# Optimization experiments

Measured on AMD Instinct MI355X. Metric: run time of the kernel, lower is better.

Reference implementation:

```python
import jax, jax.numpy as jnp
import numpy as np

NUM_EMBEDDINGS = 1024
EMBEDDING_DIM = 256
COMMITMENT_COST = 1.0


def setup_inputs() -> dict:
    key = jax.random.key(0)
    k_in, k_emb = jax.random.split(key)
    inputs = jax.random.normal(k_in, (64, 32, 32, EMBEDDING_DIM), dtype=jnp.float32)
    embeddings = jax.random.normal(k_emb, (NUM_EMBEDDINGS, EMBEDDING_DIM), dtype=jnp.float32)
    return {"inputs": inputs, "embeddings": embeddings}


def reference(inputs, embeddings):
    # Eval-mode forward of VectorQuantizerEMA (EMA buffer update is a no-grad
    # stateful side effect, skipped here; see notes).
    input_shape = inputs.shape
    flat = inputs.reshape(-1, EMBEDDING_DIM)                       # [N, D]
    distances = (
        jnp.sum(flat ** 2, axis=1, keepdims=True)
        + jnp.sum(embeddings ** 2, axis=1)
        - 2.0 * flat @ embeddings.T
    )
    encoding_indices = jnp.argmin(distances, axis=1)               # [N]
    # one-hot @ embeddings == gather (avoid materializing [N, K] one-hot)
    quantized = embeddings[encoding_indices].reshape(input_shape)
    e_latent_loss = jnp.mean((jax.lax.stop_gradient(quantized) - inputs) ** 2)
    loss = COMMITMENT_COST * e_latent_loss
    # straight-through estimator
    quantized_st = inputs + jax.lax.stop_gradient(quantized - inputs)
    return quantized_st, loss, encoding_indices[:, None]
```

## Files before the change

### kernel.cpp

```cpp
#include <hip/hip_runtime.h>
#include <float.h>

#define NROWS 65536
#define DK 256
#define NCODES 1024
#define FLAG_CAP 8192
#define MARGIN1 0.15f
#define D_BIAS 384.0f

#define LOSS_OFF 16777216
#define IDX_OFF  16777217

#define CHUNK_STRIDE 1040

#define WS_FLAG1   0
#define WS_LOSSP   8
#define WS_ENORMD  520
#define WS_ENORMF  8720
#define WS_FROWS   12816
#define WS_IDX     45584
#define WS_EHI     307728
#define WS_ET      307728

typedef _Float16 f16x8 __attribute__((ext_vector_type(8)));
typedef float f32x4 __attribute__((ext_vector_type(4)));
typedef unsigned int uint32;

__device__ __forceinline__ uint32 packh2(float a, float b) {
  return (uint32)__builtin_bit_cast(unsigned short, (_Float16)a) |
         ((uint32)__builtin_bit_cast(unsigned short, (_Float16)b) << 16);
}

__global__ __launch_bounds__(256) void init_kernel(
    const float* __restrict__ E, double* __restrict__ enorm_d,
    float* __restrict__ enorm_f, uint4* __restrict__ Ehi,
    int* __restrict__ flag1, double* __restrict__ loss_part) {
  const int t = threadIdx.x;
  const int c = blockIdx.x * 8 + (t >> 5);
  const int g = t & 31;
  if (blockIdx.x == 0) {
    if (t == 0) *flag1 = 0;
    if (t < 64) loss_part[t] = 0.0;
  }
  const float4* er4 = (const float4*)(E + (size_t)c * DK);
  const float4 va = er4[g * 2];
  const float4 vb = er4[g * 2 + 1];
  double s = (double)va.x * va.x + (double)va.y * va.y + (double)va.z * va.z + (double)va.w * va.w
           + (double)vb.x * vb.x + (double)vb.y * vb.y + (double)vb.z * vb.z + (double)vb.w * vb.w;
  uint4 h;
  h.x = packh2(va.x, va.y);
  h.y = packh2(va.z, va.w);
  h.z = packh2(vb.x, vb.y);
  h.w = packh2(vb.z, vb.w);
  const int ctg = c >> 8, cga = (c >> 4) & 15, col = c & 15;
  const int kc = g >> 2, quad = g & 3;
  Ehi[((size_t)((ctg * 8 + kc) * 16 + cga)) * 64 + (size_t)(quad * 16 + col)] = h;
  #pragma unroll
  for (int m = 1; m < 32; m <<= 1) s += __shfl_xor(s, m, 64);
  if (g == 0) {
    enorm_d[c] = s;
    enorm_f[c] = (float)s;
  }
}

__global__ __launch_bounds__(256, 3) void dist_core(
    const float* __restrict__ X, const uint4* __restrict__ Ehi,
    const float* __restrict__ enorm_f, int* __restrict__ idx_ws,
    int* __restrict__ flag1, int* __restrict__ flag_rows,
    float* __restrict__ out) {
  __shared__ __attribute__((aligned(16))) char lds[33280];
  const int tid = threadIdx.x;
  const int lane = tid & 63;
  const int wid = tid >> 6;
  const int col = lane & 15;
  const int rowBase = blockIdx.x * 64;

  {
    const float4* X4 = (const float4*)X + (size_t)rowBase * 64;
    #pragma unroll
    for (int i = 0; i < 16; ++i) {
      const int f4 = i * 256 + tid;
      const int row = f4 >> 6;
      const int k0 = (f4 & 63) << 2;
      const float4 v = X4[f4];
      uint2 p;
      p.x = packh2(v.x, v.y);
      p.y = packh2(v.z, v.w);
      const int chunk = (row >> 4) * 8 + (k0 >> 5);
      const int off = chunk * CHUNK_STRIDE
                      + (((k0 >> 3) & 3) * 16 + (row & 15)) * 16
                      + ((k0 >> 2) & 1) * 8;
      *(uint2*)(lds + off) = p;
    }
  }
  __syncthreads();

  float rv1[16], rv2[16];
  #pragma unroll
  for (int i = 0; i < 16; ++i) { rv1[i] = FLT_MAX; rv2[i] = FLT_MAX; }

  f32x4 acc[4][4];
  #pragma unroll
  for (int rg = 0; rg < 4; ++rg)
    #pragma unroll
    for (int cg = 0; cg < 4; ++cg) acc[rg][cg] = (f32x4){0.f, 0.f, 0.f, 0.f};

  f16x8 bhA[4], bhB[4];
  auto loadB_ = [&](int t, f16x8* bh) {
    const size_t ub = ((size_t)(t * 16 + wid * 4)) * 64 + (size_t)lane;
    #pragma unroll
    for (int cg = 0; cg < 4; ++cg) bh[cg] = *(const f16x8*)&Ehi[ub + (size_t)cg * 64];
  };
  auto loadA_ = [&](int t, f16x8* av) {
    const int ks = t & 7;
    #pragma unroll
    for (int rg = 0; rg < 4; ++rg)
      av[rg] = *(const f16x8*)(lds + (rg * 8 + ks) * CHUNK_STRIDE + lane * 16);
  };
  auto domfma = [&](f16x8* av, f16x8* bh) {
    #pragma unroll
    for (int rg = 0; rg < 4; ++rg)
      #pragma unroll
      for (int cg = 0; cg < 4; ++cg)
        acc[rg][cg] = __builtin_amdgcn_mfma_f32_16x16x32_f16(av[rg], bh[cg], acc[rg][cg], 0, 0, 0);
  };
  auto epilogue = [&](int ctg) {
    #pragma unroll
    for (int cg = 0; cg < 4; ++cg) {
      const int code = ctg * 256 + wid * 64 + cg * 16 + col;
      const float en = enorm_f[code] + D_BIAS;
      const uint32 li = (uint32)((ctg << 6) | (cg << 4) | col);
      #pragma unroll
      for (int rg = 0; rg < 4; ++rg)
        #pragma unroll
        for (int reg = 0; reg < 4; ++reg) {
          const int i = rg * 4 + reg;
          const float dd = fmaf(-2.0f, acc[rg][cg][reg], en);
          const float p = __builtin_bit_cast(float,
              (__builtin_bit_cast(uint32, dd) & 0xFFFFFF00u) | li);
          rv2[i] = __builtin_amdgcn_fmed3f(p, rv1[i], rv2[i]);
          rv1[i] = fminf(rv1[i], p);
        }
    }
    #pragma unroll
    for (int rg = 0; rg < 4; ++rg)
      #pragma unroll
      for (int cg = 0; cg < 4; ++cg) acc[rg][cg] = (f32x4){0.f, 0.f, 0.f, 0.f};
  };

  loadB_(0, bhA);
  f16x8 av[4];
  for (int tt = 0; tt < 32; tt += 2) {
    loadB_(tt + 1, bhB);
    loadA_(tt, av);
    domfma(av, bhA);
    if (tt + 2 < 32) loadB_(tt + 2, bhA);
    loadA_(tt + 1, av);
    domfma(av, bhB);
    if (((tt + 1) & 7) == 7) epilogue(tt >> 3);
  }

  #pragma unroll
  for (int i = 0; i < 16; ++i) {
    #pragma unroll
    for (int m = 1; m < 16; m <<= 1) {
      const float o1 = __shfl_xor(rv1[i], m, 64);
      const float o2 = __shfl_xor(rv2[i], m, 64);
      rv2[i] = fminf(fminf(rv2[i], o2), fmaxf(rv1[i], o1));
      rv1[i] = fminf(rv1[i], o1);
    }
  }

  __syncthreads();
  float* M = (float*)lds;
  if (col == 0) {
    const int quad = lane >> 4;
    #pragma unroll
    for (int i = 0; i < 16; ++i) {
      const int row = (i >> 2) * 16 + quad * 4 + (i & 3);
      M[(row * 4 + wid) * 2 + 0] = rv1[i];
      M[(row * 4 + wid) * 2 + 1] = rv2[i];
    }
  }
  __syncthreads();
  if (tid < 64) {
    const float a1 = M[(tid * 4 + 0) * 2], a2 = M[(tid * 4 + 0) * 2 + 1];
    const float b1 = M[(tid * 4 + 1) * 2], b2 = M[(tid * 4 + 1) * 2 + 1];
    const float c1 = M[(tid * 4 + 2) * 2], c2 = M[(tid * 4 + 2) * 2 + 1];
    const float d1 = M[(tid * 4 + 3) * 2], d2 = M[(tid * 4 + 3) * 2 + 1];
    const float lo1 = fminf(a1, b1), hi1 = fmaxf(a1, b1);
    const float lo2 = fminf(c1, d1), hi2 = fmaxf(c1, d1);
    const float r1 = fminf(lo1, lo2);
    const float s1 = fminf(fmaxf(lo1, lo2), fminf(hi1, hi2));
    const float r2 = fminf(fminf(fminf(a2, b2), fminf(c2, d2)), s1);
    const int w1 = (r1 == a1) ? 0 : (r1 == b1) ? 1 : (r1 == c1) ? 2 : 3;
    const uint32 u1 = __builtin_bit_cast(uint32, r1);
    const int li = (int)(u1 & 255u);
    const int code = ((li >> 6) & 3) * 256 + w1 * 64 + ((li >> 4) & 3) * 16 + (li & 15);
    const int row = rowBase + tid;
    idx_ws[row] = code;
    out[IDX_OFF + row] = (float)code;
    const float q1 = __builtin_bit_cast(float, u1 & 0xFFFFFF00u);
    const float q2 = __builtin_bit_cast(float, __builtin_bit_cast(uint32, r2) & 0xFFFFFF00u);
    if (q2 - q1 < MARGIN1) {
      const int p = atomicAdd(flag1, 1);
      if (p < FLAG_CAP) flag_rows[p] = row;
    }
  }
}

__global__ __launch_bounds__(256) void gather_out(
    const float* __restrict__ X, const float* __restrict__ E,
    const int* __restrict__ idx_ws, float* __restrict__ out,
    double* __restrict__ loss_part) {
  const int lane = threadIdx.x & 63;
  const int wid = threadIdx.x >> 6;
  const int gw = blockIdx.x * 4 + wid;
  const int nw = gridDim.x * 4;
  double ls = 0.0;
  #pragma unroll 2
  for (int row = gw; row < NROWS; row += nw) {
    const int idx = idx_ws[row];
    const float4 q = ((const float4*)E)[(size_t)idx * 64 + lane];
    const float4 x = ((const float4*)X)[(size_t)row * 64 + lane];
    ((float4*)out)[(size_t)row * 64 + lane] = q;
    const double d0 = (double)q.x - (double)x.x;
    const double d1 = (double)q.y - (double)x.y;
    const double d2 = (double)q.z - (double)x.z;
    const double d3 = (double)q.w - (double)x.w;
    ls += d0 * d0 + d1 * d1 + d2 * d2 + d3 * d3;
  }
  #pragma unroll
  for (int o = 32; o > 0; o >>= 1) ls += __shfl_down(ls, o, 64);
  __shared__ double wsum[4];
  if (lane == 0) wsum[wid] = ls;
  __syncthreads();
  if (threadIdx.x == 0)
    atomicAdd(&loss_part[blockIdx.x & 63], wsum[0] + wsum[1] + wsum[2] + wsum[3]);
}

__global__ __launch_bounds__(256) void transposeE(
    const float* __restrict__ E, float* __restrict__ Et) {
  __shared__ float tile[64][65];
  const int t = threadIdx.x;
  const int c0 = (blockIdx.x & 15) * 64;
  const int k0 = (blockIdx.x >> 4) * 64;
  {
    const int c = t & 63, q = t >> 6;
    const float4* src = (const float4*)(E + (size_t)(c0 + c) * DK + k0 + q * 16);
    #pragma unroll
    for (int j = 0; j < 4; ++j) {
      const float4 v = src[j];
      const int kk = q * 16 + j * 4;
      tile[kk + 0][c] = v.x;
      tile[kk + 1][c] = v.y;
      tile[kk + 2][c] = v.z;
      tile[kk + 3][c] = v.w;
    }
  }
  __syncthreads();
  {
    const int kk = t >> 2, cq = (t & 3) * 16;
    float4* dst = (float4*)(Et + (size_t)(k0 + kk) * NCODES + c0 + cq);
    #pragma unroll
    for (int j = 0; j < 4; ++j) {
      dst[j] = (float4){tile[kk][cq + j * 4 + 0], tile[kk][cq + j * 4 + 1],
                        tile[kk][cq + j * 4 + 2], tile[kk][cq + j * 4 + 3]};
    }
  }
}

__global__ __launch_bounds__(256, 2) void fixup_split(
    const float* __restrict__ X, const float* __restrict__ E,
    const float* __restrict__ Et, const double* __restrict__ enorm_d,
    const int* __restrict__ flag1, const int* __restrict__ flag_rows,
    const int* __restrict__ idx_ws, float* __restrict__ out,
    double* __restrict__ loss_part) {
  __shared__ double pacc[NCODES * 3];
  __shared__ double xd[256][2];
  __shared__ double red[256];
  __shared__ double wv[4][2];
  __shared__ int wi[4][2];
  __shared__ int rowL[2], oldL[2], newsh[2];
  const int tid = threadIdx.x;
  const int lane = tid & 63, wid = tid >> 6;
  int cnt = *flag1;
  if (cnt > FLAG_CAP) cnt = FLAG_CAP;
  const int ngroups = (cnt + 1) >> 1;

  for (int g = blockIdx.x; g < ngroups; g += gridDim.x) {
    const int fbase = g * 2;
    const int nr = min(2, cnt - fbase);
    __syncthreads();
    if (tid < 2) {
      const int fi = fbase + tid;
      const int row = (tid < nr) ? flag_rows[fi] : flag_rows[fbase];
      rowL[tid] = row;
      oldL[tid] = idx_ws[row];
    }
    __syncthreads();
    xd[tid][0] = (double)X[(size_t)rowL[0] * DK + tid];
    xd[tid][1] = (double)X[(size_t)rowL[1] * DK + tid];
    __syncthreads();

    double acc[4][4][2];
    #pragma unroll
    for (int q = 0; q < 4; ++q)
      #pragma unroll
      for (int j = 0; j < 4; ++j) { acc[q][j][0] = 0.0; acc[q][j][1] = 0.0; }
    const f32x4* Et4 = (const f32x4*)Et;
    #pragma unroll 2
    for (int kk = 0; kk < 64; ++kk) {
      const int k = (wid << 6) + kk;
      f32x4 e[4];
      #pragma unroll
      for (int q = 0; q < 4; ++q)
        e[q] = Et4[(size_t)k * 256 + (lane << 2) + q];
      const double x0 = xd[k][0], x1 = xd[k][1];
      #pragma unroll
      for (int q = 0; q < 4; ++q)
        #pragma unroll
        for (int j = 0; j < 4; ++j) {
          const double ed = (double)e[q][j];
          acc[q][j][0] = fma(ed, x0, acc[q][j][0]);
          acc[q][j][1] = fma(ed, x1, acc[q][j][1]);
        }
    }
    for (int w = 0; w < 4; ++w) {
      if (wid == w) {
        #pragma unroll
        for (int q = 0; q < 4; ++q)
          #pragma unroll
          for (int j = 0; j < 4; ++j) {
            const int c = (lane << 4) + (q << 2) + j;
            if (w == 0) {
              pacc[c * 3 + 0] = acc[q][j][0];
              pacc[c * 3 + 1] = acc[q][j][1];
            } else {
              pacc[c * 3 + 0] += acc[q][j][0];
              pacc[c * 3 + 1] += acc[q][j][1];
            }
          }
      }
      __syncthreads();
    }

    double bd[2] = {1e300, 1e300};
    int bi[2] = {0x7fffffff, 0x7fffffff};
    #pragma unroll
    for (int m = 0; m < 4; ++m) {
      const int c = tid + (m << 8);
      const double en = enorm_d[c];
      #pragma unroll
      for (int r = 0; r < 2; ++r) {
        const double d = en - 2.0 * pacc[c * 3 + r];
        if (d < bd[r] || (d == bd[r] && c < bi[r])) { bd[r] = d; bi[r] = c; }
      }
    }
    #pragma unroll
    for (int r = 0; r < 2; ++r) {
      double v = bd[r];
      int i = bi[r];
      #pragma unroll
      for (int m = 1; m < 64; m <<= 1) {
        const double ov = __shfl_xor(v, m, 64);
        const int oi = __shfl_xor(i, m, 64);
        if (ov < v || (ov == v && oi < i)) { v = ov; i = oi; }
      }
      if (lane == 0) { wv[wid][r] = v; wi[wid][r] = i; }
    }
    __syncthreads();
    if (tid < 2) {
      double B = wv[0][tid];
      int I = wi[0][tid];
      #pragma unroll
      for (int w = 1; w < 4; ++w) {
        if (wv[w][tid] < B || (wv[w][tid] == B && wi[w][tid] < I)) {
          B = wv[w][tid];
          I = wi[w][tid];
        }
      }
      newsh[tid] = I;
    }
    __syncthreads();

    for (int r = 0; r < nr; ++r) {
      const int newi = newsh[r];
      const int oldi = oldL[r];
      if (newi != oldi) {
        const int row = rowL[r];
        const double x = xd[tid][r];
        const float ev = E[(size_t)newi * DK + tid];
        const float eo = E[(size_t)oldi * DK + tid];
        out[(size_t)row * DK + tid] = ev;
        const double dn = (double)ev - x;
        const double dl = (double)eo - x;
        red[tid] = dn * dn - dl * dl;
        __syncthreads();
        for (int off = 128; off > 0; off >>= 1) {
          if (tid < off) red[tid] += red[tid + off];
          __syncthreads();
        }
        if (tid == 0) {
          out[IDX_OFF + row] = (float)newi;
          atomicAdd(&loss_part[row & 63], red[0]);
        }
        __syncthreads();
      }
    }
  }
}

__global__ __launch_bounds__(64) void finalize(
    const double* __restrict__ loss_part, float* __restrict__ out) {
  double v = loss_part[threadIdx.x];
  for (int o = 32; o > 0; o >>= 1) v += __shfl_down(v, o, 64);
  if (threadIdx.x == 0) out[LOSS_OFF] = (float)(v / 16777216.0);
}

extern "C" void kernel_launch(void* const* d_in, const int* in_sizes, int n_in,
                              void* d_out, int out_size, void* d_ws, size_t ws_size,
                              hipStream_t stream) {
  const float* X = (const float*)d_in[0];
  const float* E = (const float*)d_in[1];
  float* out = (float*)d_out;
  char* ws = (char*)d_ws;

  int*    flag1     = (int*)(ws + WS_FLAG1);
  double* loss_part = (double*)(ws + WS_LOSSP);
  double* enorm_d   = (double*)(ws + WS_ENORMD);
  float*  enorm_f   = (float*)(ws + WS_ENORMF);
  int*    flag_rows = (int*)(ws + WS_FROWS);
  int*    idx_ws    = (int*)(ws + WS_IDX);
  uint4*  Ehi       = (uint4*)(ws + WS_EHI);
  float*  Et        = (float*)(ws + WS_ET);

  hipLaunchKernelGGL(init_kernel, dim3(128), dim3(256), 0, stream,
                     E, enorm_d, enorm_f, Ehi, flag1, loss_part);
  hipLaunchKernelGGL(dist_core, dim3(NROWS / 64), dim3(256), 0, stream,
                     X, Ehi, enorm_f, idx_ws, flag1, flag_rows, out);
  hipLaunchKernelGGL(gather_out, dim3(2048), dim3(256), 0, stream,
                     X, E, idx_ws, out, loss_part);
  hipLaunchKernelGGL(transposeE, dim3(64), dim3(256), 0, stream, E, Et);
  hipLaunchKernelGGL(fixup_split, dim3(FLAG_CAP / 2), dim3(256), 0, stream,
                     X, E, Et, enorm_d, flag1, flag_rows, idx_ws, out, loss_part);
  hipLaunchKernelGGL(finalize, dim3(1), dim3(64), 0, stream, loss_part, out);
}
```

Measured before the change: 211.5 us.

## Deepen B-operand prefetch in dist_core and fold E transpose into gather kernel

The distance kernel's main loop now keeps four B-operand register buffers and two A buffers, so global loads are issued three tiles ahead of the MFMAs instead of one. To make room for the extra registers, the occupancy hint drops from 3 to 2 blocks per SM. The separate embedding-transpose kernel is merged into gather_out as 64 extra blocks, which removes one kernel launch and lets the transpose overlap the gather. The risk is that lower occupancy costs more latency hiding than the deeper prefetch gains, and the larger LDS tile is now reserved in every gather block.

```diff
diff --git a/kernel.cpp b/kernel.cpp
--- a/kernel.cpp
+++ b/kernel.cpp
@@ -63,7 +63,7 @@
   }
 }
 
-__global__ __launch_bounds__(256, 3) void dist_core(
+__global__ __launch_bounds__(256, 2) void dist_core(
     const float* __restrict__ X, const uint4* __restrict__ Ehi,
     const float* __restrict__ enorm_f, int* __restrict__ idx_ws,
     int* __restrict__ flag1, int* __restrict__ flag_rows,
@@ -105,7 +105,8 @@
     #pragma unroll
     for (int cg = 0; cg < 4; ++cg) acc[rg][cg] = (f32x4){0.f, 0.f, 0.f, 0.f};
 
-  f16x8 bhA[4], bhB[4];
+  f16x8 bh0[4], bh1[4], bh2[4], bh3[4];
+  f16x8 av0[4], av1[4];
   auto loadB_ = [&](int t, f16x8* bh) {
     const size_t ub = ((size_t)(t * 16 + wid * 4)) * 64 + (size_t)lane;
     #pragma unroll
@@ -148,16 +149,26 @@
       for (int cg = 0; cg < 4; ++cg) acc[rg][cg] = (f32x4){0.f, 0.f, 0.f, 0.f};
   };
 
-  loadB_(0, bhA);
-  f16x8 av[4];
-  for (int tt = 0; tt < 32; tt += 2) {
-    loadB_(tt + 1, bhB);
-    loadA_(tt, av);
-    domfma(av, bhA);
-    if (tt + 2 < 32) loadB_(tt + 2, bhA);
-    loadA_(tt + 1, av);
-    domfma(av, bhB);
-    if (((tt + 1) & 7) == 7) epilogue(tt >> 3);
+  loadB_(0, bh0);
+  loadB_(1, bh1);
+  loadB_(2, bh2);
+  loadA_(0, av0);
+  #pragma unroll
+  for (int t = 0; t < 8; ++t) {
+    const int tt = t * 4;
+    loadB_(tt + 3, bh3);
+    loadA_(tt + 1, av1);
+    domfma(av0, bh0);
+    if (tt + 4 < 32) loadB_(tt + 4, bh0);
+    loadA_(tt + 2, av0);
+    domfma(av1, bh1);
+    if (tt + 5 < 32) loadB_(tt + 5, bh1);
+    loadA_(tt + 3, av1);
+    domfma(av0, bh2);
+    if (tt + 6 < 32) loadB_(tt + 6, bh2);
+    if (tt + 4 < 32) loadA_(tt + 4, av0);
+    domfma(av1, bh3);
+    if ((t & 1) == 1) epilogue(t >> 1);
   }
 
   #pragma unroll
@@ -212,11 +223,43 @@
 __global__ __launch_bounds__(256) void gather_out(
     const float* __restrict__ X, const float* __restrict__ E,
     const int* __restrict__ idx_ws, float* __restrict__ out,
-    double* __restrict__ loss_part) {
+    double* __restrict__ loss_part, float* __restrict__ Et) {
+  __shared__ float tile[64][65];
+  __shared__ double wsum[4];
+  if (blockIdx.x >= 2048) {
+    const int bid = blockIdx.x - 2048;
+    const int t = threadIdx.x;
+    const int c0 = (bid & 15) * 64;
+    const int k0 = (bid >> 4) * 64;
+    {
+      const int c = t & 63, q = t >> 6;
+      const float4* src = (const float4*)(E + (size_t)(c0 + c) * DK + k0 + q * 16);
+      #pragma unroll
+      for (int j = 0; j < 4; ++j) {
+        const float4 v = src[j];
+        const int kk = q * 16 + j * 4;
+        tile[kk + 0][c] = v.x;
+        tile[kk + 1][c] = v.y;
+        tile[kk + 2][c] = v.z;
+        tile[kk + 3][c] = v.w;
+      }
+    }
+    __syncthreads();
+    {
+      const int kk = t >> 2, cq = (t & 3) * 16;
+      float4* dst = (float4*)(Et + (size_t)(k0 + kk) * NCODES + c0 + cq);
+      #pragma unroll
+      for (int j = 0; j < 4; ++j) {
+        dst[j] = (float4){tile[kk][cq + j * 4 + 0], tile[kk][cq + j * 4 + 1],
+                          tile[kk][cq + j * 4 + 2], tile[kk][cq + j * 4 + 3]};
+      }
+    }
+    return;
+  }
   const int lane = threadIdx.x & 63;
   const int wid = threadIdx.x >> 6;
   const int gw = blockIdx.x * 4 + wid;
-  const int nw = gridDim.x * 4;
+  const int nw = 2048 * 4;
   double ls = 0.0;
   #pragma unroll 2
   for (int row = gw; row < NROWS; row += nw) {
@@ -232,42 +275,10 @@
   }
   #pragma unroll
   for (int o = 32; o > 0; o >>= 1) ls += __shfl_down(ls, o, 64);
-  __shared__ double wsum[4];
   if (lane == 0) wsum[wid] = ls;
   __syncthreads();
   if (threadIdx.x == 0)
     atomicAdd(&loss_part[blockIdx.x & 63], wsum[0] + wsum[1] + wsum[2] + wsum[3]);
-}
-
-__global__ __launch_bounds__(256) void transposeE(
-    const float* __restrict__ E, float* __restrict__ Et) {
-  __shared__ float tile[64][65];
-  const int t = threadIdx.x;
-  const int c0 = (blockIdx.x & 15) * 64;
-  const int k0 = (blockIdx.x >> 4) * 64;
-  {
-    const int c = t & 63, q = t >> 6;
-    const float4* src = (const float4*)(E + (size_t)(c0 + c) * DK + k0 + q * 16);
-    #pragma unroll
-    for (int j = 0; j < 4; ++j) {
-      const float4 v = src[j];
-      const int kk = q * 16 + j * 4;
-      tile[kk + 0][c] = v.x;
-      tile[kk + 1][c] = v.y;
-      tile[kk + 2][c] = v.z;
-      tile[kk + 3][c] = v.w;
-    }
-  }
-  __syncthreads();
-  {
-    const int kk = t >> 2, cq = (t & 3) * 16;
-    float4* dst = (float4*)(Et + (size_t)(k0 + kk) * NCODES + c0 + cq);
-    #pragma unroll
-    for (int j = 0; j < 4; ++j) {
-      dst[j] = (float4){tile[kk][cq + j * 4 + 0], tile[kk][cq + j * 4 + 1],
-                        tile[kk][cq + j * 4 + 2], tile[kk][cq + j * 4 + 3]};
-    }
-  }
 }
 
 __global__ __launch_bounds__(256, 2) void fixup_split(
@@ -439,9 +450,8 @@
                      E, enorm_d, enorm_f, Ehi, flag1, loss_part);
   hipLaunchKernelGGL(dist_core, dim3(NROWS / 64), dim3(256), 0, stream,
                      X, Ehi, enorm_f, idx_ws, flag1, flag_rows, out);
-  hipLaunchKernelGGL(gather_out, dim3(2048), dim3(256), 0, stream,
-                     X, E, idx_ws, out, loss_part);
-  hipLaunchKernelGGL(transposeE, dim3(64), dim3(256), 0, stream, E, Et);
+  hipLaunchKernelGGL(gather_out, dim3(2112), dim3(256), 0, stream,
+                     X, E, idx_ws, out, loss_part, Et);
   hipLaunchKernelGGL(fixup_split, dim3(FLAG_CAP / 2), dim3(256), 0, stream,
                      X, E, Et, enorm_d, flag1, flag_rows, idx_ws, out, loss_part);
   hipLaunchKernelGGL(finalize, dim3(1), dim3(64), 0, stream, loss_part, out);
```

After: 271.3 us. 1.28x slower.
